# Performance work log

Measured on AMD Instinct MI355X. Metric: run time of the kernel, lower is better.

The kernel has to match this reference:

```python
import jax, jax.numpy as jnp
import numpy as np

N_NODES = 30000
N_EDGES = 480000
N_GRAPHS = 64
IN_DIM = 128
HID = 64
NEG_SLOPE = 0.2  # PyG GATConv default leaky_relu slope


def setup_inputs() -> dict:
    key = jax.random.key(0)
    ks = jax.random.split(key, 16)
    x = jax.random.normal(ks[0], (N_NODES, IN_DIM), dtype=jnp.float32)
    src = jax.random.randint(ks[1], (N_EDGES,), 0, N_NODES, dtype=jnp.int32)
    dst = jax.random.randint(ks[2], (N_EDGES,), 0, N_NODES, dtype=jnp.int32)
    edge_index = jnp.stack([src, dst], axis=0)
    # evenly-sized sorted graph assignment so every graph id is populated
    batch = (jnp.arange(N_NODES, dtype=jnp.int32) * N_GRAPHS) // N_NODES
    sc1 = 1.0 / np.sqrt(IN_DIM)
    sc2 = 1.0 / np.sqrt(4 * HID)
    sc3 = 1.0 / np.sqrt(HID)
    return dict(
        x=x, edge_index=edge_index, batch=batch,
        W1=jax.random.normal(ks[3], (IN_DIM, 4 * HID), jnp.float32) * sc1,
        att_src1=jax.random.normal(ks[4], (4, HID), jnp.float32) * sc3,
        att_dst1=jax.random.normal(ks[5], (4, HID), jnp.float32) * sc3,
        b1=jnp.zeros((4 * HID,), jnp.float32),
        W2=jax.random.normal(ks[6], (4 * HID, HID), jnp.float32) * sc2,
        att_src2=jax.random.normal(ks[7], (1, HID), jnp.float32) * sc3,
        att_dst2=jax.random.normal(ks[8], (1, HID), jnp.float32) * sc3,
        b2=jnp.zeros((HID,), jnp.float32),
        w_fc1=jax.random.normal(ks[9], (HID, HID), jnp.float32) * sc3,
        b_fc1=jnp.zeros((HID,), jnp.float32),
        w_fc2=jax.random.normal(ks[10], (HID, 2), jnp.float32) * sc3,
        b_fc2=jnp.zeros((2,), jnp.float32),
    )


def _leaky_relu(v):
    return jnp.where(v > 0, v, NEG_SLOPE * v)


def _gat_conv(x, src, dst, W, att_src, att_dst, bias, heads, ch):
    n = x.shape[0]
    h = (x @ W).reshape(n, heads, ch)                      # [N,H,C]
    a_src = jnp.sum(h * att_src[None], axis=-1)            # [N,H]
    a_dst = jnp.sum(h * att_dst[None], axis=-1)            # [N,H]
    e = _leaky_relu(a_src[src] + a_dst[dst])               # [E,H]
    e_max = jax.ops.segment_max(e, dst, num_segments=n)
    e = jnp.exp(e - e_max[dst])
    denom = jax.ops.segment_sum(e, dst, num_segments=n)
    alpha = e / denom[dst]                                 # [E,H]
    msg = h[src] * alpha[:, :, None]                       # [E,H,C]
    out = jax.ops.segment_sum(msg, dst, num_segments=n)    # [N,H,C]
    return out.reshape(n, heads * ch) + bias


def reference(x, edge_index, batch, W1, att_src1, att_dst1, b1,
              W2, att_src2, att_dst2, b2, w_fc1, b_fc1, w_fc2, b_fc2):
    n = x.shape[0]
    # add self-loops (PyG GATConv default)
    loops = jnp.arange(n, dtype=edge_index.dtype)
    src = jnp.concatenate([edge_index[0], loops])
    dst = jnp.concatenate([edge_index[1], loops])
    h = jax.nn.relu(_gat_conv(x, src, dst, W1, att_src1, att_dst1, b1, 4, HID))
    h = jax.nn.relu(_gat_conv(h, src, dst, W2, att_src2, att_dst2, b2, 1, HID))
    g = jax.ops.segment_max(h, batch, num_segments=N_GRAPHS)  # global_max_pool [G,HID]
    g = jax.nn.relu(g @ w_fc1 + b_fc1)
    logits = g @ w_fc2 + b_fc2
    return jax.nn.log_softmax(logits, axis=1)
```

## Files before the change

kernel.cpp:

```cpp
#include <hip/hip_runtime.h>
#include <hip/hip_bf16.h>
#include <math.h>

#define N_NODES  30000
#define N_EDGESR 480000
#define E_TOT    (N_EDGESR + N_NODES)
#define N_GRAPHS 64
#define IN_DIM   128
#define HID      64
#define NEG_SLOPE 0.2f

typedef __attribute__((ext_vector_type(8))) short bf16x8;
typedef __attribute__((ext_vector_type(4))) float f32x4;

__device__ __forceinline__ float lrelu(float v) { return v > 0.f ? v : NEG_SLOPE * v; }
__device__ __forceinline__ float bf2f(unsigned short u) { return __uint_as_float((unsigned)u << 16); }
__device__ __forceinline__ unsigned short f2bf(float f) {
    return __bfloat16_as_ushort(__float2bfloat16(f));
}

__global__ void zero_kernel(int* __restrict__ counts, unsigned* __restrict__ g) {
    int t = blockIdx.x * 256 + threadIdx.x;
    if (t < N_NODES) counts[t] = 0;
    if (t < N_GRAPHS * HID) g[t] = 0u;
}

__global__ void conv_x_kernel(const float* __restrict__ x, unsigned short* __restrict__ xb) {
    int i = (blockIdx.x * 256 + threadIdx.x) * 4;
    float4 v = *reinterpret_cast<const float4*>(x + i);
    ushort4 o;
    o.x = f2bf(v.x); o.y = f2bf(v.y); o.z = f2bf(v.z); o.w = f2bf(v.w);
    *reinterpret_cast<ushort4*>(xb + i) = o;
}

__global__ void conv_w_kernel(const float* __restrict__ W1, const float* __restrict__ W2,
                              unsigned short* __restrict__ w1t, unsigned short* __restrict__ w2t) {
    int id = blockIdx.x * 256 + threadIdx.x;
    if (id < 128 * 256) {
        int k = id >> 8, n = id & 255;
        w1t[n * 128 + k] = f2bf(W1[id]);
    } else {
        int id2 = id - 128 * 256;
        int k = id2 >> 6, n = id2 & 63;
        w2t[n * 256 + k] = f2bf(W2[id2]);
    }
}

__global__ void edge_hist(const int* __restrict__ ei, int* __restrict__ counts) {
    int e = blockIdx.x * blockDim.x + threadIdx.x;
    if (e >= E_TOT) return;
    int d = (e < N_EDGESR) ? ei[N_EDGESR + e] : (e - N_EDGESR);
    atomicAdd(&counts[d], 1);
}

__global__ __launch_bounds__(1024) void scan_counts(const int* __restrict__ counts,
                                                    int* __restrict__ rowstart,
                                                    int* __restrict__ cursor) {
    __shared__ int bufA[1024];
    __shared__ int bufB[1024];
    const int t = threadIdx.x;
    const int CH = 30;
    int local[CH];
    int base = t * CH;
    int s = 0;
    #pragma unroll
    for (int i = 0; i < CH; ++i) {
        int idx = base + i;
        int c = (idx < N_NODES) ? counts[idx] : 0;
        local[i] = c; s += c;
    }
    bufA[t] = s;
    __syncthreads();
    int* a = bufA; int* b = bufB;
    for (int off = 1; off < 1024; off <<= 1) {
        int v = a[t] + ((t >= off) ? a[t - off] : 0);
        b[t] = v;
        __syncthreads();
        int* tmp = a; a = b; b = tmp;
    }
    int run = (t == 0) ? 0 : a[t - 1];
    #pragma unroll
    for (int i = 0; i < CH; ++i) {
        int idx = base + i;
        if (idx < N_NODES) { rowstart[idx] = run; cursor[idx] = run; run += local[i]; }
    }
    if (t == 0) rowstart[N_NODES] = E_TOT;
}

__global__ void edge_scatter(const int* __restrict__ ei, int* __restrict__ cursor,
                             int* __restrict__ srcidx) {
    int e = blockIdx.x * blockDim.x + threadIdx.x;
    if (e >= E_TOT) return;
    int s, d;
    if (e < N_EDGESR) { s = ei[e]; d = ei[N_EDGESR + e]; }
    else              { s = d = e - N_EDGESR; }
    int pos = atomicAdd(&cursor[d], 1);
    srcidx[pos] = s;
}

__global__ __launch_bounds__(256) void mfma_gemm1(const unsigned short* __restrict__ xb,
                                                  const unsigned short* __restrict__ w1t,
                                                  unsigned short* __restrict__ h1,
                                                  const float* __restrict__ att_src,
                                                  const float* __restrict__ att_dst,
                                                  float* __restrict__ a_src,
                                                  float* __restrict__ a_dst) {
    __shared__ __align__(16) unsigned short As[64 * 128];
    const int tid = threadIdx.x;
    const int w = tid >> 6;
    const int l = tid & 63;
    const int rowbase = blockIdx.x * 64;
    char* Ab = (char*)As;

    #pragma unroll
    for (int i = 0; i < 4; ++i) {
        int flat = i * 256 + tid;
        int r = flat >> 4;
        int cb = (flat & 15) * 16;
        int gr = rowbase + r; if (gr >= N_NODES) gr = N_NODES - 1;
        int4 v = *reinterpret_cast<const int4*>(xb + (size_t)gr * 128 + (cb >> 1));
        *reinterpret_cast<int4*>(Ab + r * 256 + (cb ^ ((r & 7) << 4))) = v;
    }
    __syncthreads();

    const int lm = l & 15, lh = l >> 4;
    f32x4 acc[4][4];
    #pragma unroll
    for (int rt = 0; rt < 4; ++rt)
        #pragma unroll
        for (int ct = 0; ct < 4; ++ct)
            acc[rt][ct] = (f32x4){0.f, 0.f, 0.f, 0.f};

    #pragma unroll
    for (int s = 0; s < 4; ++s) {
        bf16x8 bfr[4], afr[4];
        #pragma unroll
        for (int ct = 0; ct < 4; ++ct) {
            int n = w * 64 + ct * 16 + lm;
            bfr[ct] = *reinterpret_cast<const bf16x8*>(w1t + n * 128 + s * 32 + lh * 8);
        }
        #pragma unroll
        for (int rt = 0; rt < 4; ++rt) {
            int row = rt * 16 + lm;
            int cb = s * 64 + lh * 16;
            afr[rt] = *reinterpret_cast<const bf16x8*>(Ab + row * 256 + (cb ^ ((row & 7) << 4)));
        }
        #pragma unroll
        for (int rt = 0; rt < 4; ++rt)
            #pragma unroll
            for (int ct = 0; ct < 4; ++ct)
                acc[rt][ct] = __builtin_amdgcn_mfma_f32_16x16x32_bf16(bfr[ct], afr[rt], acc[rt][ct], 0, 0, 0);
    }

    #pragma unroll
    for (int rt = 0; rt < 4; ++rt) {
        int row = rowbase + rt * 16 + lm;
        float ps = 0.f, pd = 0.f;
        #pragma unroll
        for (int ct = 0; ct < 4; ++ct) {
            int col = w * 64 + ct * 16 + lh * 4;
            if (row < N_NODES) {
                ushort4 o;
                o.x = f2bf(acc[rt][ct][0]); o.y = f2bf(acc[rt][ct][1]);
                o.z = f2bf(acc[rt][ct][2]); o.w = f2bf(acc[rt][ct][3]);
                *reinterpret_cast<ushort4*>(h1 + (size_t)row * 256 + col) = o;
            }
            #pragma unroll
            for (int q = 0; q < 4; ++q) {
                ps += acc[rt][ct][q] * att_src[col + q];
                pd += acc[rt][ct][q] * att_dst[col + q];
            }
        }
        ps += __shfl_xor(ps, 16); ps += __shfl_xor(ps, 32);
        pd += __shfl_xor(pd, 16); pd += __shfl_xor(pd, 32);
        if (lh == 0 && row < N_NODES) {
            a_src[row * 4 + w] = ps;
            a_dst[row * 4 + w] = pd;
        }
    }
}

__global__ __launch_bounds__(256) void mfma_gemm2(const unsigned short* __restrict__ a1b,
                                                  const unsigned short* __restrict__ w2t,
                                                  unsigned short* __restrict__ h2,
                                                  const float* __restrict__ att_src,
                                                  const float* __restrict__ att_dst,
                                                  float* __restrict__ a_src,
                                                  float* __restrict__ a_dst) {
    __shared__ __align__(16) unsigned short As[64 * 256];
    __shared__ float ps_s[4][64], pd_s[4][64];
    const int tid = threadIdx.x;
    const int w = tid >> 6, l = tid & 63;
    const int rowbase = blockIdx.x * 64;
    char* Ab = (char*)As;

    #pragma unroll
    for (int i = 0; i < 8; ++i) {
        int flat = i * 256 + tid;
        int r = flat >> 5;
        int cb = (flat & 31) * 16;
        int gr = rowbase + r; if (gr >= N_NODES) gr = N_NODES - 1;
        int4 v = *reinterpret_cast<const int4*>(a1b + (size_t)gr * 256 + (cb >> 1));
        *reinterpret_cast<int4*>(Ab + r * 512 + (cb ^ ((r & 7) << 4))) = v;
    }
    __syncthreads();

    const int lm = l & 15, lh = l >> 4;
    f32x4 acc[4];
    #pragma unroll
    for (int rt = 0; rt < 4; ++rt) acc[rt] = (f32x4){0.f, 0.f, 0.f, 0.f};

    #pragma unroll
    for (int s = 0; s < 8; ++s) {
        int n = w * 16 + lm;
        bf16x8 bf = *reinterpret_cast<const bf16x8*>(w2t + n * 256 + s * 32 + lh * 8);
        #pragma unroll
        for (int rt = 0; rt < 4; ++rt) {
            int row = rt * 16 + lm;
            int cb = s * 64 + lh * 16;
            bf16x8 af = *reinterpret_cast<const bf16x8*>(Ab + row * 512 + (cb ^ ((row & 7) << 4)));
            acc[rt] = __builtin_amdgcn_mfma_f32_16x16x32_bf16(bf, af, acc[rt], 0, 0, 0);
        }
    }

    #pragma unroll
    for (int rt = 0; rt < 4; ++rt) {
        int row = rowbase + rt * 16 + lm;
        int col = w * 16 + lh * 4;
        float ps = 0.f, pd = 0.f;
        if (row < N_NODES) {
            ushort4 o;
            o.x = f2bf(acc[rt][0]); o.y = f2bf(acc[rt][1]);
            o.z = f2bf(acc[rt][2]); o.w = f2bf(acc[rt][3]);
            *reinterpret_cast<ushort4*>(h2 + (size_t)row * 64 + col) = o;
        }
        #pragma unroll
        for (int q = 0; q < 4; ++q) {
            ps += acc[rt][q] * att_src[col + q];
            pd += acc[rt][q] * att_dst[col + q];
        }
        ps += __shfl_xor(ps, 16); ps += __shfl_xor(ps, 32);
        pd += __shfl_xor(pd, 16); pd += __shfl_xor(pd, 32);
        if (lh == 0) { ps_s[w][rt * 16 + lm] = ps; pd_s[w][rt * 16 + lm] = pd; }
    }
    __syncthreads();
    if (tid < 64) {
        int row = rowbase + tid;
        if (row < N_NODES) {
            a_src[row] = ps_s[0][tid] + ps_s[1][tid] + ps_s[2][tid] + ps_s[3][tid];
            a_dst[row] = pd_s[0][tid] + pd_s[1][tid] + pd_s[2][tid] + pd_s[3][tid];
        }
    }
}

__global__ __launch_bounds__(256) void gat_agg1(const unsigned short* __restrict__ h1,
                                                const float* __restrict__ a_src,
                                                const float* __restrict__ a_dst,
                                                const int* __restrict__ rowstart,
                                                const int* __restrict__ srcidx,
                                                const float* __restrict__ b1,
                                                unsigned short* __restrict__ out1) {
    int n = (blockIdx.x * 256 + threadIdx.x) >> 6;
    int lane = threadIdx.x & 63;
    if (n >= N_NODES) return;
    int beg = rowstart[n], end = rowstart[n + 1];
    const int h    = lane & 3;
    const int slot = lane >> 2;
    const int myhead = lane >> 4;
    float ad_h = a_dst[n * 4 + h];

    float4 acc = make_float4(0.f, 0.f, 0.f, 0.f);
    float den_part = 0.f;
    int cb = beg;
    for (; cb + 16 <= end; cb += 16) {
        int s = srcidx[cb + slot];
        float w = __expf(lrelu(a_src[s * 4 + h] + ad_h));
        den_part += w;
        #pragma unroll
        for (int j = 0; j < 16; ++j) {
            float wj = __shfl(w, j * 4 + myhead);
            int   sj = __shfl(s, j * 4);
            ushort4 hv = *reinterpret_cast<const ushort4*>(&h1[(size_t)sj * 256 + lane * 4]);
            acc.x += wj * bf2f(hv.x); acc.y += wj * bf2f(hv.y);
            acc.z += wj * bf2f(hv.z); acc.w += wj * bf2f(hv.w);
        }
    }
    if (cb < end) {
        int cnt = end - cb;
        float w = 0.f; int s = 0;
        if (slot < cnt) {
            s = srcidx[cb + slot];
            w = __expf(lrelu(a_src[s * 4 + h] + ad_h));
            den_part += w;
        }
        for (int j = 0; j < cnt; ++j) {
            float wj = __shfl(w, j * 4 + myhead);
            int   sj = __shfl(s, j * 4);
            ushort4 hv = *reinterpret_cast<const ushort4*>(&h1[(size_t)sj * 256 + lane * 4]);
            acc.x += wj * bf2f(hv.x); acc.y += wj * bf2f(hv.y);
            acc.z += wj * bf2f(hv.z); acc.w += wj * bf2f(hv.w);
        }
    }
    #pragma unroll
    for (int off = 4; off < 64; off <<= 1) den_part += __shfl_xor(den_part, off);
    float den = __shfl(den_part, myhead);
    float inv = 1.f / den;
    float4 bv = *reinterpret_cast<const float4*>(&b1[lane * 4]);
    ushort4 o;
    o.x = f2bf(fmaxf(acc.x * inv + bv.x, 0.f));
    o.y = f2bf(fmaxf(acc.y * inv + bv.y, 0.f));
    o.z = f2bf(fmaxf(acc.z * inv + bv.z, 0.f));
    o.w = f2bf(fmaxf(acc.w * inv + bv.w, 0.f));
    *reinterpret_cast<ushort4*>(&out1[(size_t)n * 256 + lane * 4]) = o;
}

__global__ __launch_bounds__(256) void gat_agg2_pool(const unsigned short* __restrict__ h2,
                                                     const float* __restrict__ a_src,
                                                     const float* __restrict__ a_dst,
                                                     const int* __restrict__ rowstart,
                                                     const int* __restrict__ srcidx,
                                                     const float* __restrict__ b2,
                                                     const int* __restrict__ batch,
                                                     unsigned* __restrict__ g) {
    __shared__ float sm[4][64];
    const int wid = threadIdx.x >> 6;
    const int lane = threadIdx.x & 63;
    const int n = blockIdx.x * 4 + wid;
    const int grp = lane >> 4;
    const int cl  = lane & 15;
    int beg = rowstart[n], end = rowstart[n + 1];
    float ad = a_dst[n];

    float4 acc = make_float4(0.f, 0.f, 0.f, 0.f);
    float den_part = 0.f;
    int cb = beg;
    for (; cb + 16 <= end; cb += 16) {
        float w = 0.f; int s = 0;
        if (lane < 16) {
            s = srcidx[cb + lane];
            w = __expf(lrelu(a_src[s] + ad));
            den_part += w;
        }
        #pragma unroll
        for (int j = 0; j < 16; j += 4) {
            float wj = __shfl(w, j + grp);
            int   sj = __shfl(s, j + grp);
            ushort4 hv = *reinterpret_cast<const ushort4*>(&h2[(size_t)sj * 64 + cl * 4]);
            acc.x += wj * bf2f(hv.x); acc.y += wj * bf2f(hv.y);
            acc.z += wj * bf2f(hv.z); acc.w += wj * bf2f(hv.w);
        }
    }
    if (cb < end) {
        int cnt = end - cb;
        float w = 0.f; int s = 0;
        if (lane < cnt) {
            s = srcidx[cb + lane];
            w = __expf(lrelu(a_src[s] + ad));
            den_part += w;
        }
        for (int j = 0; j < cnt; j += 4) {
            float wj = __shfl(w, j + grp);
            int   sj = __shfl(s, j + grp);
            if (j + grp < cnt) {
                ushort4 hv = *reinterpret_cast<const ushort4*>(&h2[(size_t)sj * 64 + cl * 4]);
                acc.x += wj * bf2f(hv.x); acc.y += wj * bf2f(hv.y);
                acc.z += wj * bf2f(hv.z); acc.w += wj * bf2f(hv.w);
            }
        }
    }
    #pragma unroll
    for (int off = 16; off < 64; off <<= 1) {
        acc.x += __shfl_xor(acc.x, off);
        acc.y += __shfl_xor(acc.y, off);
        acc.z += __shfl_xor(acc.z, off);
        acc.w += __shfl_xor(acc.w, off);
    }
    #pragma unroll
    for (int off = 1; off < 64; off <<= 1) den_part += __shfl_xor(den_part, off);
    float inv = 1.f / den_part;
    float4 bv = *reinterpret_cast<const float4*>(&b2[cl * 4]);
    if (lane < 16) {
        float4 val;
        val.x = fmaxf(acc.x * inv + bv.x, 0.f);
        val.y = fmaxf(acc.y * inv + bv.y, 0.f);
        val.z = fmaxf(acc.z * inv + bv.z, 0.f);
        val.w = fmaxf(acc.w * inv + bv.w, 0.f);
        *reinterpret_cast<float4*>(&sm[wid][cl * 4]) = val;
    }
    __syncthreads();
    int b0 = batch[blockIdx.x * 4];
    int b3 = batch[blockIdx.x * 4 + 3];
    if (b0 == b3) {
        if (threadIdx.x < 64) {
            float v = fmaxf(fmaxf(sm[0][threadIdx.x], sm[1][threadIdx.x]),
                            fmaxf(sm[2][threadIdx.x], sm[3][threadIdx.x]));
            atomicMax(&g[b0 * 64 + threadIdx.x], __float_as_uint(v));
        }
    } else {
        if (lane < 16) {
            int bb = batch[n];
            #pragma unroll
            for (int k = 0; k < 4; ++k)
                atomicMax(&g[bb * 64 + cl * 4 + k], __float_as_uint(sm[wid][cl * 4 + k]));
        }
    }
}

__global__ __launch_bounds__(256) void head_kernel(const float* __restrict__ g,
                                                   const float* __restrict__ w_fc1,
                                                   const float* __restrict__ b_fc1,
                                                   const float* __restrict__ w_fc2,
                                                   const float* __restrict__ b_fc2,
                                                   float* __restrict__ out) {
    __shared__ float gs[64][65];
    __shared__ float hs[64][65];
    int t = threadIdx.x;
    #pragma unroll
    for (int it = 0; it < 16; ++it) {
        int flat = it * 256 + t;
        gs[flat >> 6][flat & 63] = g[flat];
    }
    __syncthreads();
    #pragma unroll
    for (int it = 0; it < 16; ++it) {
        int flat = it * 256 + t;
        int i = flat >> 6, j = flat & 63;
        float s = b_fc1[j];
        #pragma unroll 8
        for (int k = 0; k < 64; ++k) s += gs[i][k] * w_fc1[k * 64 + j];
        hs[i][j] = fmaxf(s, 0.f);
    }
    __syncthreads();
    if (t < 64) {
        float l0 = b_fc2[0], l1 = b_fc2[1];
        #pragma unroll 8
        for (int k = 0; k < 64; ++k) {
            float v = hs[t][k];
            l0 += v * w_fc2[k * 2];
            l1 += v * w_fc2[k * 2 + 1];
        }
        float mx = fmaxf(l0, l1);
        float lse = mx + logf(__expf(l0 - mx) + __expf(l1 - mx));
        out[t * 2]     = l0 - lse;
        out[t * 2 + 1] = l1 - lse;
    }
}

extern "C" void kernel_launch(void* const* d_in, const int* in_sizes, int n_in,
                              void* d_out, int out_size, void* d_ws, size_t ws_size,
                              hipStream_t stream) {
    const float* x        = (const float*)d_in[0];
    const int*   ei       = (const int*)d_in[1];
    const int*   batch    = (const int*)d_in[2];
    const float* W1       = (const float*)d_in[3];
    const float* att_src1 = (const float*)d_in[4];
    const float* att_dst1 = (const float*)d_in[5];
    const float* b1       = (const float*)d_in[6];
    const float* W2       = (const float*)d_in[7];
    const float* att_src2 = (const float*)d_in[8];
    const float* att_dst2 = (const float*)d_in[9];
    const float* b2       = (const float*)d_in[10];
    const float* w_fc1    = (const float*)d_in[11];
    const float* b_fc1    = (const float*)d_in[12];
    const float* w_fc2    = (const float*)d_in[13];
    const float* b_fc2    = (const float*)d_in[14];

    char* ws = (char*)d_ws;
    size_t off = 0;
    auto alloc = [&](size_t bytes) -> char* {
        char* p = ws + off;
        off += (bytes + 255) & ~(size_t)255;
        return p;
    };
    unsigned short* xb   = (unsigned short*)alloc((size_t)N_NODES * 128 * 2);
    unsigned short* w1t  = (unsigned short*)alloc((size_t)256 * 128 * 2);
    unsigned short* w2t  = (unsigned short*)alloc((size_t)64 * 256 * 2);
    unsigned short* h1   = (unsigned short*)alloc((size_t)N_NODES * 256 * 2);
    unsigned short* out1 = (unsigned short*)alloc((size_t)N_NODES * 256 * 2);
    unsigned short* h2   = (unsigned short*)alloc((size_t)N_NODES * 64 * 2);
    float*    as1        = (float*)alloc((size_t)N_NODES * 4 * 4);
    float*    ad1        = (float*)alloc((size_t)N_NODES * 4 * 4);
    float*    as2        = (float*)alloc((size_t)N_NODES * 4);
    float*    ad2        = (float*)alloc((size_t)N_NODES * 4);
    int*      counts     = (int*)alloc((size_t)N_NODES * 4);
    int*      rowstart   = (int*)alloc((size_t)(N_NODES + 4) * 4);
    int*      cursor     = (int*)alloc((size_t)(N_NODES + 4) * 4);
    int*      srcidx     = (int*)alloc((size_t)E_TOT * 4);
    unsigned* g          = (unsigned*)alloc((size_t)N_GRAPHS * HID * 4);

    zero_kernel<<<(N_NODES + 255) / 256, 256, 0, stream>>>(counts, g);
    conv_x_kernel<<<(N_NODES * 128 / 4 + 255) / 256, 256, 0, stream>>>(x, xb);
    conv_w_kernel<<<192, 256, 0, stream>>>(W1, W2, w1t, w2t);

    edge_hist<<<(E_TOT + 255) / 256, 256, 0, stream>>>(ei, counts);
    scan_counts<<<1, 1024, 0, stream>>>(counts, rowstart, cursor);
    edge_scatter<<<(E_TOT + 255) / 256, 256, 0, stream>>>(ei, cursor, srcidx);

    mfma_gemm1<<<(N_NODES + 63) / 64, 256, 0, stream>>>(xb, w1t, h1, att_src1, att_dst1, as1, ad1);
    gat_agg1<<<7500, 256, 0, stream>>>(h1, as1, ad1, rowstart, srcidx, b1, out1);

    mfma_gemm2<<<(N_NODES + 63) / 64, 256, 0, stream>>>(out1, w2t, h2, att_src2, att_dst2, as2, ad2);
    gat_agg2_pool<<<7500, 256, 0, stream>>>(h2, as2, ad2, rowstart, srcidx, b2, batch, g);

    head_kernel<<<1, 256, 0, stream>>>((const float*)g, w_fc1, b_fc1, w_fc2, b_fc2, (float*)d_out);
}
```

Baseline: 199.4 us.

## Aggregate raw features before layer-1 projection and fold attention vectors into W1

Layer 1 now computes attention logits by precomputing W1·att vectors (p1) so per-node scores come from x directly, then aggregates 128-dim bf16 x rows per head (gather of 256B instead of 512B per edge) into a 512-wide buffer, and applies the W1 GEMM plus bias/relu afterwards. Small prep kernels are merged (conversion, zeroing, weight transpose; histogram with p1; scatter with dot products) to cut launches. The trade-off is a larger intermediate (N x 512 bf16) written and read by the GEMM, and more accumulator registers in aggregation.

```diff
diff --git a/kernel.cpp b/kernel.cpp
--- a/kernel.cpp
+++ b/kernel.cpp
@@ -11,6 +11,7 @@
 #define NEG_SLOPE 0.2f
 
 typedef __attribute__((ext_vector_type(8))) short bf16x8;
+typedef __attribute__((ext_vector_type(8))) unsigned short u16x8;
 typedef __attribute__((ext_vector_type(4))) float f32x4;
 
 __device__ __forceinline__ float lrelu(float v) { return v > 0.f ? v : NEG_SLOPE * v; }
@@ -19,38 +20,58 @@
     return __bfloat16_as_ushort(__float2bfloat16(f));
 }
 
-__global__ void zero_kernel(int* __restrict__ counts, unsigned* __restrict__ g) {
+__global__ __launch_bounds__(256) void prep_kernel(const float* __restrict__ x,
+                                                   const float* __restrict__ W1,
+                                                   const float* __restrict__ W2,
+                                                   unsigned short* __restrict__ xb,
+                                                   unsigned short* __restrict__ w1t,
+                                                   unsigned short* __restrict__ w2t,
+                                                   int* __restrict__ counts,
+                                                   unsigned* __restrict__ g) {
     int t = blockIdx.x * 256 + threadIdx.x;
-    if (t < N_NODES) counts[t] = 0;
-    if (t < N_GRAPHS * HID) g[t] = 0u;
-}
-
-__global__ void conv_x_kernel(const float* __restrict__ x, unsigned short* __restrict__ xb) {
-    int i = (blockIdx.x * 256 + threadIdx.x) * 4;
-    float4 v = *reinterpret_cast<const float4*>(x + i);
-    ushort4 o;
-    o.x = f2bf(v.x); o.y = f2bf(v.y); o.z = f2bf(v.z); o.w = f2bf(v.w);
-    *reinterpret_cast<ushort4*>(xb + i) = o;
-}
-
-__global__ void conv_w_kernel(const float* __restrict__ W1, const float* __restrict__ W2,
-                              unsigned short* __restrict__ w1t, unsigned short* __restrict__ w2t) {
-    int id = blockIdx.x * 256 + threadIdx.x;
-    if (id < 128 * 256) {
+    if (t < 480000) {
+        int i = t * 8;
+        float4 v0 = *reinterpret_cast<const float4*>(x + i);
+        float4 v1 = *reinterpret_cast<const float4*>(x + i + 4);
+        u16x8 o;
+        o[0] = f2bf(v0.x); o[1] = f2bf(v0.y); o[2] = f2bf(v0.z); o[3] = f2bf(v0.w);
+        o[4] = f2bf(v1.x); o[5] = f2bf(v1.y); o[6] = f2bf(v1.z); o[7] = f2bf(v1.w);
+        *reinterpret_cast<u16x8*>(xb + i) = o;
+    } else if (t < 510000) {
+        counts[t - 480000] = 0;
+    } else if (t < 514096) {
+        g[t - 510000] = 0u;
+    } else if (t < 546864) {
+        int id = t - 514096;
         int k = id >> 8, n = id & 255;
         w1t[n * 128 + k] = f2bf(W1[id]);
+    } else if (t < 563248) {
+        int id = t - 546864;
+        int k = id >> 6, n = id & 63;
+        w2t[n * 256 + k] = f2bf(W2[id]);
+    }
+}
+
+__global__ void edge_hist_p1(const int* __restrict__ ei, int* __restrict__ counts,
+                             const float* __restrict__ W1,
+                             const float* __restrict__ att_src, const float* __restrict__ att_dst,
+                             float* __restrict__ p1) {
+    int t = blockIdx.x * 256 + threadIdx.x;
+    if (t < E_TOT) {
+        int d = (t < N_EDGESR) ? ei[N_EDGESR + t] : (t - N_EDGESR);
+        atomicAdd(&counts[d], 1);
     } else {
-        int id2 = id - 128 * 256;
-        int k = id2 >> 6, n = id2 & 63;
-        w2t[n * 256 + k] = f2bf(W2[id2]);
-    }
-}
-
-__global__ void edge_hist(const int* __restrict__ ei, int* __restrict__ counts) {
-    int e = blockIdx.x * blockDim.x + threadIdx.x;
-    if (e >= E_TOT) return;
-    int d = (e < N_EDGESR) ? ei[N_EDGESR + e] : (e - N_EDGESR);
-    atomicAdd(&counts[d], 1);
+        int id = t - E_TOT;
+        if (id < 1024) {
+            int k = id >> 3, j = id & 7;
+            const float* av = (j < 4) ? (att_src + j * 64) : (att_dst + (j - 4) * 64);
+            const float* wrow = W1 + k * 256 + (j & 3) * 64;
+            float s = 0.f;
+            #pragma unroll 8
+            for (int c = 0; c < 64; ++c) s += wrow[c] * av[c];
+            p1[id] = s;
+        }
+    }
 }
 
 __global__ __launch_bounds__(1024) void scan_counts(const int* __restrict__ counts,
@@ -87,43 +108,134 @@
     if (t == 0) rowstart[N_NODES] = E_TOT;
 }
 
-__global__ void edge_scatter(const int* __restrict__ ei, int* __restrict__ cursor,
-                             int* __restrict__ srcidx) {
-    int e = blockIdx.x * blockDim.x + threadIdx.x;
-    if (e >= E_TOT) return;
-    int s, d;
-    if (e < N_EDGESR) { s = ei[e]; d = ei[N_EDGESR + e]; }
-    else              { s = d = e - N_EDGESR; }
-    int pos = atomicAdd(&cursor[d], 1);
-    srcidx[pos] = s;
-}
-
-__global__ __launch_bounds__(256) void mfma_gemm1(const unsigned short* __restrict__ xb,
-                                                  const unsigned short* __restrict__ w1t,
-                                                  unsigned short* __restrict__ h1,
-                                                  const float* __restrict__ att_src,
-                                                  const float* __restrict__ att_dst,
-                                                  float* __restrict__ a_src,
-                                                  float* __restrict__ a_dst) {
-    __shared__ __align__(16) unsigned short As[64 * 128];
+#define SCAT_BLOCKS 1993
+__global__ __launch_bounds__(256) void edge_scatter_dots(const int* __restrict__ ei,
+                                                         int* __restrict__ cursor,
+                                                         int* __restrict__ srcidx,
+                                                         const unsigned short* __restrict__ xb,
+                                                         const float* __restrict__ p1,
+                                                         float* __restrict__ as1,
+                                                         float* __restrict__ ad1) {
+    if (blockIdx.x < SCAT_BLOCKS) {
+        int e = blockIdx.x * 256 + threadIdx.x;
+        if (e >= E_TOT) return;
+        int s, d;
+        if (e < N_EDGESR) { s = ei[e]; d = ei[N_EDGESR + e]; }
+        else              { s = d = e - N_EDGESR; }
+        int pos = atomicAdd(&cursor[d], 1);
+        srcidx[pos] = s;
+    } else {
+        int n = (blockIdx.x - SCAT_BLOCKS) * 4 + (threadIdx.x >> 6);
+        int lane = threadIdx.x & 63;
+        if (n >= N_NODES) return;
+        ushort2 xv = *reinterpret_cast<const ushort2*>(xb + (size_t)n * 128 + 2 * lane);
+        float x0 = bf2f(xv.x), x1 = bf2f(xv.y);
+        const float* pp = p1 + 16 * lane;
+        float4 p0a = *reinterpret_cast<const float4*>(pp);
+        float4 p0b = *reinterpret_cast<const float4*>(pp + 4);
+        float4 p1a = *reinterpret_cast<const float4*>(pp + 8);
+        float4 p1b = *reinterpret_cast<const float4*>(pp + 12);
+        float f[8];
+        f[0] = x0 * p0a.x + x1 * p1a.x; f[1] = x0 * p0a.y + x1 * p1a.y;
+        f[2] = x0 * p0a.z + x1 * p1a.z; f[3] = x0 * p0a.w + x1 * p1a.w;
+        f[4] = x0 * p0b.x + x1 * p1b.x; f[5] = x0 * p0b.y + x1 * p1b.y;
+        f[6] = x0 * p0b.z + x1 * p1b.z; f[7] = x0 * p0b.w + x1 * p1b.w;
+        #pragma unroll
+        for (int off = 1; off < 64; off <<= 1) {
+            #pragma unroll
+            for (int q = 0; q < 8; ++q) f[q] += __shfl_xor(f[q], off);
+        }
+        if (lane < 4)      as1[n * 4 + lane] = f[lane];
+        else if (lane < 8) ad1[n * 4 + lane - 4] = f[lane];
+    }
+}
+
+__global__ __launch_bounds__(256) void gat_agg1x(const unsigned short* __restrict__ xb,
+                                                 const float* __restrict__ as1,
+                                                 const float* __restrict__ ad1,
+                                                 const int* __restrict__ rowstart,
+                                                 const int* __restrict__ srcidx,
+                                                 unsigned short* __restrict__ aggb) {
+    int n = (blockIdx.x * 256 + threadIdx.x) >> 6;
+    int lane = threadIdx.x & 63;
+    if (n >= N_NODES) return;
+    int beg = rowstart[n], end = rowstart[n + 1];
+    const int h = lane & 3, slot = lane >> 2;
+    const int half = lane >> 5, cl = lane & 31;
+    float ad_h = ad1[n * 4 + h];
+
+    float acc[4][4] = {};
+    float den_part = 0.f;
+    int cb = beg;
+    for (; cb + 16 <= end; cb += 16) {
+        int s = srcidx[cb + slot];
+        float w = __expf(lrelu(as1[s * 4 + h] + ad_h));
+        den_part += w;
+        #pragma unroll
+        for (int j = 0; j < 16; j += 2) {
+            int e = j + half;
+            float w0 = __shfl(w, e * 4 + 0), w1 = __shfl(w, e * 4 + 1);
+            float w2 = __shfl(w, e * 4 + 2), w3 = __shfl(w, e * 4 + 3);
+            int sj = __shfl(s, e * 4);
+            ushort4 hv = *reinterpret_cast<const ushort4*>(xb + (size_t)sj * 128 + cl * 4);
+            float x0 = bf2f(hv.x), x1 = bf2f(hv.y), x2 = bf2f(hv.z), x3 = bf2f(hv.w);
+            acc[0][0] += w0 * x0; acc[0][1] += w0 * x1; acc[0][2] += w0 * x2; acc[0][3] += w0 * x3;
+            acc[1][0] += w1 * x0; acc[1][1] += w1 * x1; acc[1][2] += w1 * x2; acc[1][3] += w1 * x3;
+            acc[2][0] += w2 * x0; acc[2][1] += w2 * x1; acc[2][2] += w2 * x2; acc[2][3] += w2 * x3;
+            acc[3][0] += w3 * x0; acc[3][1] += w3 * x1; acc[3][2] += w3 * x2; acc[3][3] += w3 * x3;
+        }
+    }
+    if (cb < end) {
+        int cnt = end - cb;
+        int s = srcidx[(slot < cnt) ? (cb + slot) : beg];
+        float w = 0.f;
+        if (slot < cnt) { w = __expf(lrelu(as1[s * 4 + h] + ad_h)); den_part += w; }
+        for (int j = 0; j < cnt; j += 2) {
+            int e = j + half;
+            float w0 = __shfl(w, e * 4 + 0), w1 = __shfl(w, e * 4 + 1);
+            float w2 = __shfl(w, e * 4 + 2), w3 = __shfl(w, e * 4 + 3);
+            int sj = __shfl(s, e * 4);
+            if (e < cnt) {
+                ushort4 hv = *reinterpret_cast<const ushort4*>(xb + (size_t)sj * 128 + cl * 4);
+                float x0 = bf2f(hv.x), x1 = bf2f(hv.y), x2 = bf2f(hv.z), x3 = bf2f(hv.w);
+                acc[0][0] += w0 * x0; acc[0][1] += w0 * x1; acc[0][2] += w0 * x2; acc[0][3] += w0 * x3;
+                acc[1][0] += w1 * x0; acc[1][1] += w1 * x1; acc[1][2] += w1 * x2; acc[1][3] += w1 * x3;
+                acc[2][0] += w2 * x0; acc[2][1] += w2 * x1; acc[2][2] += w2 * x2; acc[2][3] += w2 * x3;
+                acc[3][0] += w3 * x0; acc[3][1] += w3 * x1; acc[3][2] += w3 * x2; acc[3][3] += w3 * x3;
+            }
+        }
+    }
+    #pragma unroll
+    for (int hh = 0; hh < 4; ++hh)
+        #pragma unroll
+        for (int q = 0; q < 4; ++q)
+            acc[hh][q] += __shfl_xor(acc[hh][q], 32);
+    #pragma unroll
+    for (int off = 4; off < 64; off <<= 1) den_part += __shfl_xor(den_part, off);
+    float inv[4];
+    inv[0] = 1.f / __shfl(den_part, 0);
+    inv[1] = 1.f / __shfl(den_part, 1);
+    inv[2] = 1.f / __shfl(den_part, 2);
+    inv[3] = 1.f / __shfl(den_part, 3);
+    int hb = half * 2;
+    #pragma unroll
+    for (int k = 0; k < 2; ++k) {
+        int hh = hb + k;
+        ushort4 o;
+        o.x = f2bf(acc[hh][0] * inv[hh]); o.y = f2bf(acc[hh][1] * inv[hh]);
+        o.z = f2bf(acc[hh][2] * inv[hh]); o.w = f2bf(acc[hh][3] * inv[hh]);
+        *reinterpret_cast<ushort4*>(aggb + (size_t)n * 512 + hh * 128 + cl * 4) = o;
+    }
+}
+
+__global__ __launch_bounds__(256) void mfma_gemm1b(const unsigned short* __restrict__ aggb,
+                                                   const unsigned short* __restrict__ w1t,
+                                                   const float* __restrict__ b1,
+                                                   unsigned short* __restrict__ out1) {
     const int tid = threadIdx.x;
-    const int w = tid >> 6;
-    const int l = tid & 63;
+    const int w = tid >> 6, l = tid & 63;
+    const int lm = l & 15, lh = l >> 4;
     const int rowbase = blockIdx.x * 64;
-    char* Ab = (char*)As;
-
-    #pragma unroll
-    for (int i = 0; i < 4; ++i) {
-        int flat = i * 256 + tid;
-        int r = flat >> 4;
-        int cb = (flat & 15) * 16;
-        int gr = rowbase + r; if (gr >= N_NODES) gr = N_NODES - 1;
-        int4 v = *reinterpret_cast<const int4*>(xb + (size_t)gr * 128 + (cb >> 1));
-        *reinterpret_cast<int4*>(Ab + r * 256 + (cb ^ ((r & 7) << 4))) = v;
-    }
-    __syncthreads();
-
-    const int lm = l & 15, lh = l >> 4;
     f32x4 acc[4][4];
     #pragma unroll
     for (int rt = 0; rt < 4; ++rt)
@@ -136,14 +248,14 @@
         bf16x8 bfr[4], afr[4];
         #pragma unroll
         for (int ct = 0; ct < 4; ++ct) {
-            int n = w * 64 + ct * 16 + lm;
-            bfr[ct] = *reinterpret_cast<const bf16x8*>(w1t + n * 128 + s * 32 + lh * 8);
+            int col = w * 64 + ct * 16 + lm;
+            bfr[ct] = *reinterpret_cast<const bf16x8*>(w1t + col * 128 + s * 32 + lh * 8);
         }
         #pragma unroll
         for (int rt = 0; rt < 4; ++rt) {
-            int row = rt * 16 + lm;
-            int cb = s * 64 + lh * 16;
-            afr[rt] = *reinterpret_cast<const bf16x8*>(Ab + row * 256 + (cb ^ ((row & 7) << 4)));
+            int row = rowbase + rt * 16 + lm;
+            if (row >= N_NODES) row = N_NODES - 1;
+            afr[rt] = *reinterpret_cast<const bf16x8*>(aggb + (size_t)row * 512 + w * 128 + s * 32 + lh * 8);
         }
         #pragma unroll
         for (int rt = 0; rt < 4; ++rt)
@@ -155,27 +267,17 @@
     #pragma unroll
     for (int rt = 0; rt < 4; ++rt) {
         int row = rowbase + rt * 16 + lm;
-        float ps = 0.f, pd = 0.f;
+        if (row >= N_NODES) continue;
         #pragma unroll
         for (int ct = 0; ct < 4; ++ct) {
             int col = w * 64 + ct * 16 + lh * 4;
-            if (row < N_NODES) {
-                ushort4 o;
-                o.x = f2bf(acc[rt][ct][0]); o.y = f2bf(acc[rt][ct][1]);
-                o.z = f2bf(acc[rt][ct][2]); o.w = f2bf(acc[rt][ct][3]);
-                *reinterpret_cast<ushort4*>(h1 + (size_t)row * 256 + col) = o;
-            }
-            #pragma unroll
-            for (int q = 0; q < 4; ++q) {
-                ps += acc[rt][ct][q] * att_src[col + q];
-                pd += acc[rt][ct][q] * att_dst[col + q];
-            }
-        }
-        ps += __shfl_xor(ps, 16); ps += __shfl_xor(ps, 32);
-        pd += __shfl_xor(pd, 16); pd += __shfl_xor(pd, 32);
-        if (lh == 0 && row < N_NODES) {
-            a_src[row * 4 + w] = ps;
-            a_dst[row * 4 + w] = pd;
+            float4 bv = *reinterpret_cast<const float4*>(b1 + col);
+            ushort4 o;
+            o.x = f2bf(fmaxf(acc[rt][ct][0] + bv.x, 0.f));
+            o.y = f2bf(fmaxf(acc[rt][ct][1] + bv.y, 0.f));
+            o.z = f2bf(fmaxf(acc[rt][ct][2] + bv.z, 0.f));
+            o.w = f2bf(fmaxf(acc[rt][ct][3] + bv.w, 0.f));
+            *reinterpret_cast<ushort4*>(out1 + (size_t)row * 256 + col) = o;
         }
     }
 }
@@ -251,67 +353,6 @@
             a_dst[row] = pd_s[0][tid] + pd_s[1][tid] + pd_s[2][tid] + pd_s[3][tid];
         }
     }
-}
-
-__global__ __launch_bounds__(256) void gat_agg1(const unsigned short* __restrict__ h1,
-                                                const float* __restrict__ a_src,
-                                                const float* __restrict__ a_dst,
-                                                const int* __restrict__ rowstart,
-                                                const int* __restrict__ srcidx,
-                                                const float* __restrict__ b1,
-                                                unsigned short* __restrict__ out1) {
-    int n = (blockIdx.x * 256 + threadIdx.x) >> 6;
-    int lane = threadIdx.x & 63;
-    if (n >= N_NODES) return;
-    int beg = rowstart[n], end = rowstart[n + 1];
-    const int h    = lane & 3;
-    const int slot = lane >> 2;
-    const int myhead = lane >> 4;
-    float ad_h = a_dst[n * 4 + h];
-
-    float4 acc = make_float4(0.f, 0.f, 0.f, 0.f);
-    float den_part = 0.f;
-    int cb = beg;
-    for (; cb + 16 <= end; cb += 16) {
-        int s = srcidx[cb + slot];
-        float w = __expf(lrelu(a_src[s * 4 + h] + ad_h));
-        den_part += w;
-        #pragma unroll
-        for (int j = 0; j < 16; ++j) {
-            float wj = __shfl(w, j * 4 + myhead);
-            int   sj = __shfl(s, j * 4);
-            ushort4 hv = *reinterpret_cast<const ushort4*>(&h1[(size_t)sj * 256 + lane * 4]);
-            acc.x += wj * bf2f(hv.x); acc.y += wj * bf2f(hv.y);
-            acc.z += wj * bf2f(hv.z); acc.w += wj * bf2f(hv.w);
-        }
-    }
-    if (cb < end) {
-        int cnt = end - cb;
-        float w = 0.f; int s = 0;
-        if (slot < cnt) {
-            s = srcidx[cb + slot];
-            w = __expf(lrelu(a_src[s * 4 + h] + ad_h));
-            den_part += w;
-        }
-        for (int j = 0; j < cnt; ++j) {
-            float wj = __shfl(w, j * 4 + myhead);
-            int   sj = __shfl(s, j * 4);
-            ushort4 hv = *reinterpret_cast<const ushort4*>(&h1[(size_t)sj * 256 + lane * 4]);
-            acc.x += wj * bf2f(hv.x); acc.y += wj * bf2f(hv.y);
-            acc.z += wj * bf2f(hv.z); acc.w += wj * bf2f(hv.w);
-        }
-    }
-    #pragma unroll
-    for (int off = 4; off < 64; off <<= 1) den_part += __shfl_xor(den_part, off);
-    float den = __shfl(den_part, myhead);
-    float inv = 1.f / den;
-    float4 bv = *reinterpret_cast<const float4*>(&b1[lane * 4]);
-    ushort4 o;
-    o.x = f2bf(fmaxf(acc.x * inv + bv.x, 0.f));
-    o.y = f2bf(fmaxf(acc.y * inv + bv.y, 0.f));
-    o.z = f2bf(fmaxf(acc.z * inv + bv.z, 0.f));
-    o.w = f2bf(fmaxf(acc.w * inv + bv.w, 0.f));
-    *reinterpret_cast<ushort4*>(&out1[(size_t)n * 256 + lane * 4]) = o;
 }
 
 __global__ __launch_bounds__(256) void gat_agg2_pool(const unsigned short* __restrict__ h2,
@@ -475,7 +516,8 @@
     unsigned short* xb   = (unsigned short*)alloc((size_t)N_NODES * 128 * 2);
     unsigned short* w1t  = (unsigned short*)alloc((size_t)256 * 128 * 2);
     unsigned short* w2t  = (unsigned short*)alloc((size_t)64 * 256 * 2);
-    unsigned short* h1   = (unsigned short*)alloc((size_t)N_NODES * 256 * 2);
+    float*    p1         = (float*)alloc((size_t)128 * 8 * 4);
+    unsigned short* aggb = (unsigned short*)alloc((size_t)N_NODES * 512 * 2);
     unsigned short* out1 = (unsigned short*)alloc((size_t)N_NODES * 256 * 2);
     unsigned short* h2   = (unsigned short*)alloc((size_t)N_NODES * 64 * 2);
     float*    as1        = (float*)alloc((size_t)N_NODES * 4 * 4);
@@ -488,19 +530,13 @@
     int*      srcidx     = (int*)alloc((size_t)E_TOT * 4);
     unsigned* g          = (unsigned*)alloc((size_t)N_GRAPHS * HID * 4);
 
-    zero_kernel<<<(N_NODES + 255) / 256, 256, 0, stream>>>(counts, g);
-    conv_x_kernel<<<(N_NODES * 128 / 4 + 255) / 256, 256, 0, stream>>>(x, xb);
-    conv_w_kernel<<<192, 256, 0, stream>>>(W1, W2, w1t, w2t);
-
-    edge_hist<<<(E_TOT + 255) / 256, 256, 0, stream>>>(ei, counts);
+    prep_kernel<<<2201, 256, 0, stream>>>(x, W1, W2, xb, w1t, w2t, counts, g);
+    edge_hist_p1<<<1997, 256, 0, stream>>>(ei, counts, W1, att_src1, att_dst1, p1);
     scan_counts<<<1, 1024, 0, stream>>>(counts, rowstart, cursor);
-    edge_scatter<<<(E_TOT + 255) / 256, 256, 0, stream>>>(ei, cursor, srcidx);
-
-    mfma_gemm1<<<(N_NODES + 63) / 64, 256, 0, stream>>>(xb, w1t, h1, att_src1, att_dst1, as1, ad1);
-    gat_agg1<<<7500, 256, 0, stream>>>(h1, as1, ad1, rowstart, srcidx, b1, out1);
-
+    edge_scatter_dots<<<SCAT_BLOCKS + 7500, 256, 0, stream>>>(ei, cursor, srcidx, xb, p1, as1, ad1);
+    gat_agg1x<<<7500, 256, 0, stream>>>(xb, as1, ad1, rowstart, srcidx, aggb);
+    mfma_gemm1b<<<(N_NODES + 63) / 64, 256, 0, stream>>>(aggb, w1t, b1, out1);
     mfma_gemm2<<<(N_NODES + 63) / 64, 256, 0, stream>>>(out1, w2t, h2, att_src2, att_dst2, as2, ad2);
     gat_agg2_pool<<<7500, 256, 0, stream>>>(h2, as2, ad2, rowstart, srcidx, b2, batch, g);
-
     head_kernel<<<1, 256, 0, stream>>>((const float*)g, w_fc1, b_fc1, w_fc2, b_fc2, (float*)d_out);
 }
```

Measured after the change: 255.4 us. 28.1% more time.
